# Performance work log

Measured on AMD Instinct MI355X. Metric: run time of the kernel, lower is better.

## Reference

```python
import jax, jax.numpy as jnp
import numpy as np

B, S, D, F, H, E = 4, 1024, 512, 2048, 8, 8
LN_EPS = 1e-5


def setup_inputs() -> dict:
    key = jax.random.key(0)
    ks = jax.random.split(key, 8)
    sd = 1.0 / np.sqrt(D)
    return {
        'x': jax.random.normal(ks[0], (B, S, D), jnp.float32),
        'in_proj_w': jax.random.normal(ks[1], (3 * D, D), jnp.float32) * sd,
        'in_proj_b': jnp.zeros((3 * D,), jnp.float32),
        'out_proj_w': jax.random.normal(ks[2], (D, D), jnp.float32) * sd,
        'out_proj_b': jnp.zeros((D,), jnp.float32),
        'ln1_g': jnp.ones((D,), jnp.float32),
        'ln1_b': jnp.zeros((D,), jnp.float32),
        'ln2_g': jnp.ones((D,), jnp.float32),
        'ln2_b': jnp.zeros((D,), jnp.float32),
        'router_w': jax.random.normal(ks[3], (D, E), jnp.float32) * sd,
        'wi': jax.random.normal(ks[4], (E, D, F), jnp.float32) * sd,
        'wo': jax.random.normal(ks[5], (E, F, D), jnp.float32) * (1.0 / np.sqrt(F)),
        'expert_capacity': 256,
    }


def _layernorm(x, g, b):
    mu = jnp.mean(x, axis=-1, keepdims=True)
    var = jnp.var(x, axis=-1, keepdims=True)
    return (x - mu) * jax.lax.rsqrt(var + LN_EPS) * g + b


def _mha(x, in_w, in_b, out_w, out_b):
    # torch nn.MultiheadAttention, batch_first, self-attention, no mask
    qkv = x @ in_w.T + in_b                         # [B,S,3D]
    q, k, v = jnp.split(qkv, 3, axis=-1)
    hd = D // H

    def heads(t):
        return t.reshape(B, S, H, hd).transpose(0, 2, 1, 3)  # [B,H,S,hd]

    q, k, v = heads(q), heads(k), heads(v)
    scores = jnp.einsum('bhqd,bhkd->bhqk', q, k) / np.sqrt(hd)
    attn = jax.nn.softmax(scores, axis=-1)
    o = jnp.einsum('bhqk,bhkd->bhqd', attn, v)
    o = o.transpose(0, 2, 1, 3).reshape(B, S, D)
    return o @ out_w.T + out_b


def _router(x, router_w, capacity):
    # Switch-style top-1 router with per-(batch,expert) capacity
    logits = x.astype(jnp.float32) @ router_w       # [B,S,E]
    probs = jax.nn.softmax(logits, axis=-1)
    idx = jnp.argmax(probs, axis=-1)                # [B,S]
    one_hot = jax.nn.one_hot(idx, E, dtype=probs.dtype)
    pos = jnp.cumsum(one_hot, axis=1)               # position within each expert queue
    keep = one_hot * (pos <= capacity).astype(probs.dtype)
    expert_mask = keep * probs                      # dispatch mask scaled by router prob
    return expert_mask, probs, logits


def reference(x, in_proj_w, in_proj_b, out_proj_w, out_proj_b,
              ln1_g, ln1_b, ln2_g, ln2_b, router_w, wi, wo, expert_capacity):
    # self-attention block (post-norm)
    residual = x
    a = _mha(x, in_proj_w, in_proj_b, out_proj_w, out_proj_b)
    h = _layernorm(residual + a, ln1_g, ln1_b)

    # sparse MoE FFN
    expert_mask, _, router_logits = _router(h, router_w, expert_capacity)
    residual = h
    moe = jnp.zeros_like(h)
    for e in range(E):  # fixed small expert loop; masked-dense == gather/FFN/scatter
        y = jax.nn.gelu(h @ wi[e], approximate=False) @ wo[e]
        moe = moe + expert_mask[..., e:e + 1] * y

    out = _layernorm(residual + moe, ln2_g, ln2_b)
    return out, router_logits, expert_mask
```

## Files before the change

### kernel.cpp

```cpp
#include <hip/hip_runtime.h>
#include <math.h>

#define SEQ 1024
#define NTOK 4096
#define DM 512
#define FF 2048
#define NE 8

typedef __attribute__((ext_vector_type(8))) short bf16x8;
typedef __attribute__((ext_vector_type(4))) float f32x4;

__device__ __forceinline__ short f2bf(float f) {
  unsigned u = __float_as_uint(f);
  unsigned r = (u + 0x7FFFu + ((u >> 16) & 1u)) >> 16;
  return (short)r;
}
__device__ __forceinline__ float bf2f(short h) {
  return __uint_as_float(((unsigned)(unsigned short)h) << 16);
}

#define GLOAD_LDS16(g, l) __builtin_amdgcn_global_load_lds( \
    (const __attribute__((address_space(1))) void*)(g),     \
    (__attribute__((address_space(3))) void*)(l), 16, 0, 0)

__global__ __launch_bounds__(256) void split_kernel(const float* __restrict__ src,
    short* __restrict__ hi, short* __restrict__ lo) {
  const size_t base = ((size_t)blockIdx.x * 256 + threadIdx.x) * 8;
  float4 v0 = *reinterpret_cast<const float4*>(src + base);
  float4 v1 = *reinterpret_cast<const float4*>(src + base + 4);
  short h[8]; short l[8];
  float v[8] = {v0.x, v0.y, v0.z, v0.w, v1.x, v1.y, v1.z, v1.w};
#pragma unroll
  for (int i = 0; i < 8; ++i) {
    h[i] = f2bf(v[i]);
    l[i] = f2bf(v[i] - bf2f(h[i]));
  }
  *reinterpret_cast<short4*>(hi + base)     = make_short4(h[0], h[1], h[2], h[3]);
  *reinterpret_cast<short4*>(hi + base + 4) = make_short4(h[4], h[5], h[6], h[7]);
  *reinterpret_cast<short4*>(lo + base)     = make_short4(l[0], l[1], l[2], l[3]);
  *reinterpret_cast<short4*>(lo + base + 4) = make_short4(l[4], l[5], l[6], l[7]);
}

template<int BNF>
__global__ __launch_bounds__(256) void gemm_split(const short* __restrict__ Ah, const short* __restrict__ Al,
    const short* __restrict__ Bh, const short* __restrict__ Bl,
    const float* __restrict__ bias, const float* __restrict__ resid, float* __restrict__ C,
    int N, int K) {
  constexpr int BN = 32 * BNF;
  __shared__ __align__(16) short AsH[128 * 32];
  __shared__ __align__(16) short AsL[128 * 32];
  __shared__ __align__(16) short BsH[BN * 32];
  __shared__ __align__(16) short BsL[BN * 32];
  const int n0 = blockIdx.x * BN, m0 = blockIdx.y * 128;
  const int tid = threadIdx.x;
  const int lane = tid & 63, w = tid >> 6;
  const int quad = lane >> 4, l15 = lane & 15;
  const int wm = (w & 1) * 64, wn = (w >> 1) * 16 * BNF;
  const int sr = tid >> 2, sc = (tid & 3) * 8;
  const short* Ahp = Ah + (size_t)(m0 + sr) * K;
  const short* Alp = Al + (size_t)(m0 + sr) * K;
  const short* Bhp = Bh + (size_t)(n0 + sr) * K;
  const short* Blp = Bl + (size_t)(n0 + sr) * K;
  f32x4 acc[4][BNF];
#pragma unroll
  for (int i = 0; i < 4; ++i)
#pragma unroll
    for (int j = 0; j < BNF; ++j) acc[i][j] = (f32x4){0.f, 0.f, 0.f, 0.f};
  for (int kt = 0; kt < K; kt += 32) {
    GLOAD_LDS16(Ahp + kt + sc,                  &AsH[tid * 8]);
    GLOAD_LDS16(Ahp + (size_t)64 * K + kt + sc, &AsH[2048 + tid * 8]);
    GLOAD_LDS16(Alp + kt + sc,                  &AsL[tid * 8]);
    GLOAD_LDS16(Alp + (size_t)64 * K + kt + sc, &AsL[2048 + tid * 8]);
    GLOAD_LDS16(Bhp + kt + sc,                  &BsH[tid * 8]);
    GLOAD_LDS16(Blp + kt + sc,                  &BsL[tid * 8]);
    if (BNF == 4) {
      GLOAD_LDS16(Bhp + (size_t)64 * K + kt + sc, &BsH[2048 + tid * 8]);
      GLOAD_LDS16(Blp + (size_t)64 * K + kt + sc, &BsL[2048 + tid * 8]);
    }
    __syncthreads();
    bf16x8 ah[4], al[4], bh[BNF], bl[BNF];
#pragma unroll
    for (int i = 0; i < 4; ++i) {
      ah[i] = *reinterpret_cast<const bf16x8*>(&AsH[(wm + i * 16 + l15) * 32 + quad * 8]);
      al[i] = *reinterpret_cast<const bf16x8*>(&AsL[(wm + i * 16 + l15) * 32 + quad * 8]);
    }
#pragma unroll
    for (int j = 0; j < BNF; ++j) {
      bh[j] = *reinterpret_cast<const bf16x8*>(&BsH[(wn + j * 16 + l15) * 32 + quad * 8]);
      bl[j] = *reinterpret_cast<const bf16x8*>(&BsL[(wn + j * 16 + l15) * 32 + quad * 8]);
    }
#pragma unroll
    for (int i = 0; i < 4; ++i)
#pragma unroll
      for (int j = 0; j < BNF; ++j) {
        acc[i][j] = __builtin_amdgcn_mfma_f32_16x16x32_bf16(al[i], bh[j], acc[i][j], 0, 0, 0);
        acc[i][j] = __builtin_amdgcn_mfma_f32_16x16x32_bf16(ah[i], bl[j], acc[i][j], 0, 0, 0);
        acc[i][j] = __builtin_amdgcn_mfma_f32_16x16x32_bf16(ah[i], bh[j], acc[i][j], 0, 0, 0);
      }
    __syncthreads();
  }
#pragma unroll
  for (int i = 0; i < 4; ++i) {
#pragma unroll
    for (int reg = 0; reg < 4; ++reg) {
      const int row = m0 + wm + i * 16 + quad * 4 + reg;
#pragma unroll
      for (int j = 0; j < BNF; ++j) {
        const int col = n0 + wn + j * 16 + l15;
        float v = acc[i][j][reg] + bias[col];
        if (resid) v += resid[(size_t)row * N + col];
        C[(size_t)row * N + col] = v;
      }
    }
  }
}

__global__ __launch_bounds__(256) void gemm_split_qkv(const short* __restrict__ Ah, const short* __restrict__ Al,
    const short* __restrict__ Bh, const short* __restrict__ Bl, const float* __restrict__ bias,
    short* __restrict__ qkh, short* __restrict__ qkl, short* __restrict__ vh, short* __restrict__ vl) {
  const int K = DM;
  __shared__ __align__(16) short AsH[128 * 32];
  __shared__ __align__(16) short AsL[128 * 32];
  __shared__ __align__(16) short BsH[128 * 32];
  __shared__ __align__(16) short BsL[128 * 32];
  const int n0 = blockIdx.x * 128, m0 = blockIdx.y * 128;
  const int tid = threadIdx.x;
  const int lane = tid & 63, w = tid >> 6;
  const int quad = lane >> 4, l15 = lane & 15;
  const int wm = (w & 1) * 64, wn = (w >> 1) * 64;
  const int sr = tid >> 2, sc = (tid & 3) * 8;
  const short* Ahp = Ah + (size_t)(m0 + sr) * K;
  const short* Alp = Al + (size_t)(m0 + sr) * K;
  const short* Bhp = Bh + (size_t)(n0 + sr) * K;
  const short* Blp = Bl + (size_t)(n0 + sr) * K;
  f32x4 acc[4][4];
#pragma unroll
  for (int i = 0; i < 4; ++i)
#pragma unroll
    for (int j = 0; j < 4; ++j) acc[i][j] = (f32x4){0.f, 0.f, 0.f, 0.f};
  for (int kt = 0; kt < K; kt += 32) {
    GLOAD_LDS16(Ahp + kt + sc,                  &AsH[tid * 8]);
    GLOAD_LDS16(Ahp + (size_t)64 * K + kt + sc, &AsH[2048 + tid * 8]);
    GLOAD_LDS16(Alp + kt + sc,                  &AsL[tid * 8]);
    GLOAD_LDS16(Alp + (size_t)64 * K + kt + sc, &AsL[2048 + tid * 8]);
    GLOAD_LDS16(Bhp + kt + sc,                  &BsH[tid * 8]);
    GLOAD_LDS16(Bhp + (size_t)64 * K + kt + sc, &BsH[2048 + tid * 8]);
    GLOAD_LDS16(Blp + kt + sc,                  &BsL[tid * 8]);
    GLOAD_LDS16(Blp + (size_t)64 * K + kt + sc, &BsL[2048 + tid * 8]);
    __syncthreads();
    bf16x8 ah[4], al[4], bh[4], bl[4];
#pragma unroll
    for (int i = 0; i < 4; ++i) {
      ah[i] = *reinterpret_cast<const bf16x8*>(&AsH[(wm + i * 16 + l15) * 32 + quad * 8]);
      al[i] = *reinterpret_cast<const bf16x8*>(&AsL[(wm + i * 16 + l15) * 32 + quad * 8]);
      bh[i] = *reinterpret_cast<const bf16x8*>(&BsH[(wn + i * 16 + l15) * 32 + quad * 8]);
      bl[i] = *reinterpret_cast<const bf16x8*>(&BsL[(wn + i * 16 + l15) * 32 + quad * 8]);
    }
#pragma unroll
    for (int i = 0; i < 4; ++i)
#pragma unroll
      for (int j = 0; j < 4; ++j) {
        acc[i][j] = __builtin_amdgcn_mfma_f32_16x16x32_bf16(al[i], bh[j], acc[i][j], 0, 0, 0);
        acc[i][j] = __builtin_amdgcn_mfma_f32_16x16x32_bf16(ah[i], bl[j], acc[i][j], 0, 0, 0);
        acc[i][j] = __builtin_amdgcn_mfma_f32_16x16x32_bf16(ah[i], bh[j], acc[i][j], 0, 0, 0);
      }
    __syncthreads();
  }
  if (blockIdx.x < 8) {
#pragma unroll
    for (int i = 0; i < 4; ++i) {
#pragma unroll
      for (int reg = 0; reg < 4; ++reg) {
        const int row = m0 + wm + i * 16 + quad * 4 + reg;
#pragma unroll
        for (int j = 0; j < 4; ++j) {
          const int col = n0 + wn + j * 16 + l15;
          float v = acc[i][j][reg] + bias[col];
          short hv = f2bf(v);
          size_t ad = (size_t)row * 1024 + col;
          qkh[ad] = hv;
          qkl[ad] = f2bf(v - bf2f(hv));
        }
      }
    }
  } else {
#pragma unroll
    for (int i = 0; i < 4; ++i) {
      const int row0 = m0 + wm + i * 16 + quad * 4;
      const int bb = row0 >> 10, s0 = row0 & 1023;
#pragma unroll
      for (int j = 0; j < 4; ++j) {
        const int col = n0 + wn + j * 16 + l15;
        const int c2 = col - 1024;
        const int hhd = c2 >> 6, d = c2 & 63;
        const float bc = bias[col];
        float v0 = acc[i][j][0] + bc, v1 = acc[i][j][1] + bc, v2 = acc[i][j][2] + bc, v3 = acc[i][j][3] + bc;
        short4 hv = make_short4(f2bf(v0), f2bf(v1), f2bf(v2), f2bf(v3));
        short4 lv = make_short4(f2bf(v0 - bf2f(hv.x)), f2bf(v1 - bf2f(hv.y)),
                                f2bf(v2 - bf2f(hv.z)), f2bf(v3 - bf2f(hv.w)));
        size_t ad = ((size_t)(bb * 8 + hhd) * 64 + d) * 1024 + s0;
        *reinterpret_cast<short4*>(vh + ad) = hv;
        *reinterpret_cast<short4*>(vl + ad) = lv;
      }
    }
  }
}

__global__ __launch_bounds__(256) void attn_mfma(const short* __restrict__ qkh, const short* __restrict__ qkl,
    const short* __restrict__ vth, const short* __restrict__ vtl,
    short* __restrict__ oh, short* __restrict__ ol) {
  const int qt = blockIdx.x, hh = blockIdx.y, b = blockIdx.z;
  __shared__ __align__(16) short Qh[4096], Ql[4096], Kh[4096], Kl[4096], Vh[4096], Vl[4096];
  const int tid = threadIdx.x;
  const int lane = tid & 63, w = tid >> 6;
  const int quad = lane >> 4, l15 = lane & 15;
  const int tok0 = b * SEQ + qt * 64;
  const int srow = tid >> 2, schunk = (tid & 3) * 8;
  {
    const size_t qa = (size_t)(tok0 + srow) * 1024 + hh * 64 + schunk;
    GLOAD_LDS16(qkh + qa,      &Qh[tid * 8]);
    GLOAD_LDS16(qkh + qa + 32, &Qh[2048 + tid * 8]);
    GLOAD_LDS16(qkl + qa,      &Ql[tid * 8]);
    GLOAD_LDS16(qkl + qa + 32, &Ql[2048 + tid * 8]);
  }
  __syncthreads();
  bf16x8 qfh[2], qfl[2];
#pragma unroll
  for (int ks = 0; ks < 2; ++ks) {
    qfh[ks] = *reinterpret_cast<const bf16x8*>(&Qh[ks * 2048 + (w * 16 + l15) * 32 + quad * 8]);
    qfl[ks] = *reinterpret_cast<const bf16x8*>(&Ql[ks * 2048 + (w * 16 + l15) * 32 + quad * 8]);
  }
  f32x4 oacc[4];
  float m_run[4], l_run[4];
#pragma unroll
  for (int r = 0; r < 4; ++r) { oacc[r] = (f32x4){0.f, 0.f, 0.f, 0.f}; m_run[r] = -1e30f; l_run[r] = 0.f; }
  const size_t kbase = (size_t)(b * SEQ) * 1024 + 512 + hh * 64;
  const size_t vbase = (size_t)(b * 8 + hh) * 64 * 1024;
  for (int kc = 0; kc < 16; ++kc) {
    const size_t ka = kbase + (size_t)(kc * 64 + srow) * 1024 + schunk;
    GLOAD_LDS16(qkh + ka,      &Kh[tid * 8]);
    GLOAD_LDS16(qkh + ka + 32, &Kh[2048 + tid * 8]);
    GLOAD_LDS16(qkl + ka,      &Kl[tid * 8]);
    GLOAD_LDS16(qkl + ka + 32, &Kl[2048 + tid * 8]);
    const size_t va = vbase + (size_t)srow * 1024 + kc * 64 + schunk;
    GLOAD_LDS16(vth + va,      &Vh[tid * 8]);
    GLOAD_LDS16(vth + va + 32, &Vh[2048 + tid * 8]);
    GLOAD_LDS16(vtl + va,      &Vl[tid * 8]);
    GLOAD_LDS16(vtl + va + 32, &Vl[2048 + tid * 8]);
    __syncthreads();
    f32x4 s[4];
#pragma unroll
    for (int j = 0; j < 4; ++j) s[j] = (f32x4){0.f, 0.f, 0.f, 0.f};
#pragma unroll
    for (int ks = 0; ks < 2; ++ks)
#pragma unroll
      for (int j = 0; j < 4; ++j) {
        bf16x8 kfh = *reinterpret_cast<const bf16x8*>(&Kh[ks * 2048 + (j * 16 + l15) * 32 + quad * 8]);
        bf16x8 kfl = *reinterpret_cast<const bf16x8*>(&Kl[ks * 2048 + (j * 16 + l15) * 32 + quad * 8]);
        s[j] = __builtin_amdgcn_mfma_f32_16x16x32_bf16(qfl[ks], kfh, s[j], 0, 0, 0);
        s[j] = __builtin_amdgcn_mfma_f32_16x16x32_bf16(qfh[ks], kfl, s[j], 0, 0, 0);
        s[j] = __builtin_amdgcn_mfma_f32_16x16x32_bf16(qfh[ks], kfh, s[j], 0, 0, 0);
      }
    __syncthreads();
    float pv[4][4], alpha[4];
#pragma unroll
    for (int reg = 0; reg < 4; ++reg) {
      float mc = fmaxf(fmaxf(s[0][reg], s[1][reg]), fmaxf(s[2][reg], s[3][reg]));
#pragma unroll
      for (int msk = 1; msk < 16; msk <<= 1) mc = fmaxf(mc, __shfl_xor(mc, msk, 64));
      mc *= 0.125f;
      float mn = fmaxf(m_run[reg], mc);
      alpha[reg] = expf(m_run[reg] - mn);
      m_run[reg] = mn;
      float pl = 0.f;
#pragma unroll
      for (int j = 0; j < 4; ++j) { float pp = expf(s[j][reg] * 0.125f - mn); pv[j][reg] = pp; pl += pp; }
#pragma unroll
      for (int msk = 1; msk < 16; msk <<= 1) pl += __shfl_xor(pl, msk, 64);
      l_run[reg] = l_run[reg] * alpha[reg] + pl;
    }
#pragma unroll
    for (int j = 0; j < 4; ++j) {
      oacc[j][0] *= alpha[0]; oacc[j][1] *= alpha[1]; oacc[j][2] *= alpha[2]; oacc[j][3] *= alpha[3];
    }
#pragma unroll
    for (int j = 0; j < 4; ++j) {
      const int cad = (j >> 1) * 2048 + (j & 1) * 16 + l15;
#pragma unroll
      for (int reg = 0; reg < 4; ++reg) {
        const int ad = cad + (w * 16 + quad * 4 + reg) * 32;
        float p = pv[j][reg];
        short hp = f2bf(p);
        Kh[ad] = hp;
        Kl[ad] = f2bf(p - bf2f(hp));
      }
    }
#pragma unroll
    for (int ks = 0; ks < 2; ++ks) {
      bf16x8 pfh = *reinterpret_cast<const bf16x8*>(&Kh[ks * 2048 + (w * 16 + l15) * 32 + quad * 8]);
      bf16x8 pfl = *reinterpret_cast<const bf16x8*>(&Kl[ks * 2048 + (w * 16 + l15) * 32 + quad * 8]);
#pragma unroll
      for (int j = 0; j < 4; ++j) {
        bf16x8 vfh = *reinterpret_cast<const bf16x8*>(&Vh[ks * 2048 + (j * 16 + l15) * 32 + quad * 8]);
        bf16x8 vfl = *reinterpret_cast<const bf16x8*>(&Vl[ks * 2048 + (j * 16 + l15) * 32 + quad * 8]);
        oacc[j] = __builtin_amdgcn_mfma_f32_16x16x32_bf16(pfl, vfh, oacc[j], 0, 0, 0);
        oacc[j] = __builtin_amdgcn_mfma_f32_16x16x32_bf16(pfh, vfl, oacc[j], 0, 0, 0);
        oacc[j] = __builtin_amdgcn_mfma_f32_16x16x32_bf16(pfh, vfh, oacc[j], 0, 0, 0);
      }
    }
    __syncthreads();
  }
#pragma unroll
  for (int reg = 0; reg < 4; ++reg) {
    float inv = 1.f / l_run[reg];
#pragma unroll
    for (int j = 0; j < 4; ++j) {
      float v = oacc[j][reg] * inv;
      size_t ad = (size_t)(tok0 + w * 16 + quad * 4 + reg) * 512 + hh * 64 + j * 16 + l15;
      short hv = f2bf(v);
      oh[ad] = hv;
      ol[ad] = f2bf(v - bf2f(hv));
    }
  }
}

__global__ __launch_bounds__(64) void ln_kernel(const float* __restrict__ x, const float* __restrict__ add,
    const float* __restrict__ g, const float* __restrict__ bta, float* __restrict__ y) {
  const int t = blockIdx.x, tid = threadIdx.x;
  const size_t base = (size_t)t * DM + tid * 8;
  float4 v0 = *reinterpret_cast<const float4*>(x + base);
  float4 v1 = *reinterpret_cast<const float4*>(x + base + 4);
  if (add) {
    float4 a0 = *reinterpret_cast<const float4*>(add + base);
    float4 a1 = *reinterpret_cast<const float4*>(add + base + 4);
    v0.x += a0.x; v0.y += a0.y; v0.z += a0.z; v0.w += a0.w;
    v1.x += a1.x; v1.y += a1.y; v1.z += a1.z; v1.w += a1.w;
  }
  float s = v0.x+v0.y+v0.z+v0.w + v1.x+v1.y+v1.z+v1.w;
  float q = v0.x*v0.x+v0.y*v0.y+v0.z*v0.z+v0.w*v0.w + v1.x*v1.x+v1.y*v1.y+v1.z*v1.z+v1.w*v1.w;
#pragma unroll
  for (int m = 1; m < 64; m <<= 1) { s += __shfl_xor(s, m, 64); q += __shfl_xor(q, m, 64); }
  float mean = s * (1.0f/512.0f);
  float var = q * (1.0f/512.0f) - mean * mean;
  float rs = rsqrtf(var + 1e-5f);
  float4 g0 = *reinterpret_cast<const float4*>(g + tid*8);
  float4 g1 = *reinterpret_cast<const float4*>(g + tid*8 + 4);
  float4 b0 = *reinterpret_cast<const float4*>(bta + tid*8);
  float4 b1 = *reinterpret_cast<const float4*>(bta + tid*8 + 4);
  float4 o0 = make_float4((v0.x-mean)*rs*g0.x+b0.x, (v0.y-mean)*rs*g0.y+b0.y,
                          (v0.z-mean)*rs*g0.z+b0.z, (v0.w-mean)*rs*g0.w+b0.w);
  float4 o1 = make_float4((v1.x-mean)*rs*g1.x+b1.x, (v1.y-mean)*rs*g1.y+b1.y,
                          (v1.z-mean)*rs*g1.z+b1.z, (v1.w-mean)*rs*g1.w+b1.w);
  *reinterpret_cast<float4*>(y + base) = o0;
  *reinterpret_cast<float4*>(y + base + 4) = o1;
}

__global__ __launch_bounds__(256) void router_kernel(const float* __restrict__ h, const float* __restrict__ rw,
    float* __restrict__ rlog) {
  int gidx = blockIdx.x * 256 + threadIdx.x;
  int t = gidx >> 3, e = gidx & 7;
  const float* hr = h + (size_t)t * DM;
  float acc = 0.f;
#pragma unroll 8
  for (int d = 0; d < DM; ++d) acc += hr[d] * rw[d * NE + e];
  rlog[gidx] = acc;
}

__global__ __launch_bounds__(256) void smax_kernel(const float* __restrict__ rlog, float* __restrict__ probs,
    int* __restrict__ am) {
  int t = blockIdx.x * 256 + threadIdx.x;
  float v[8];
#pragma unroll
  for (int e = 0; e < 8; ++e) v[e] = rlog[t * 8 + e];
  int best = 0; float bv = v[0];
#pragma unroll
  for (int e = 1; e < 8; ++e) if (v[e] > bv) { bv = v[e]; best = e; }
  float ex[8]; float s = 0.f;
#pragma unroll
  for (int e = 0; e < 8; ++e) { ex[e] = expf(v[e] - bv); s += ex[e]; }
  float inv = 1.f / s;
#pragma unroll
  for (int e = 0; e < 8; ++e) probs[t * 8 + e] = ex[e] * inv;
  am[t] = best;
}

__global__ __launch_bounds__(256) void scan_kernel(const int* __restrict__ am, const float* __restrict__ probs,
    const int* __restrict__ capp, float* __restrict__ emask, int* __restrict__ pos, int* __restrict__ cnt) {
  const int bx = blockIdx.x;
  const int b = bx >> 3, e = bx & 7;
  const int tid = threadIdx.x;
  const int cap = *capp;
  __shared__ int arr[256];
  const int s_base = tid * 4;
  int f[4], incl[4];
  int c = 0;
#pragma unroll
  for (int i = 0; i < 4; ++i) {
    f[i] = (am[b * SEQ + s_base + i] == e) ? 1 : 0;
    c += f[i]; incl[i] = c;
  }
  arr[tid] = c;
  __syncthreads();
  for (int off = 1; off < 256; off <<= 1) {
    int v = (tid >= off) ? arr[tid - off] : 0;
    __syncthreads();
    arr[tid] += v;
    __syncthreads();
  }
  int excl = arr[tid] - c;
  int tot = arr[255];
#pragma unroll
  for (int i = 0; i < 4; ++i) {
    int token = b * SEQ + s_base + i;
    int p = excl + incl[i];
    bool kept = f[i] && (p <= cap);
    emask[(size_t)token * NE + e] = kept ? probs[token * NE + e] : 0.f;
    if (f[i]) pos[token] = p;
  }
  if (tid == 0) cnt[bx] = (tot < cap) ? tot : cap;
}

__global__ __launch_bounds__(64) void offsets_kernel(const int* __restrict__ cnt, int* __restrict__ offbe,
    int* __restrict__ total) {
  int e = threadIdx.x;
  if (e < NE) {
    int run = 0;
    for (int b = 0; b < 4; ++b) { offbe[b * NE + e] = run; run += cnt[b * NE + e]; }
    total[e] = run;
  }
}

__global__ __launch_bounds__(256) void transpose_bf16(const float* __restrict__ W, short* __restrict__ Wt,
    int K, int N) {
  __shared__ float T[32][33];
  const float* We = W + (size_t)blockIdx.z * K * N;
  short* Wte = Wt + (size_t)blockIdx.z * K * N;
  const int k0 = blockIdx.y * 32, n0 = blockIdx.x * 32;
  const int r = threadIdx.x >> 3, c4 = (threadIdx.x & 7) * 4;
  float4 v = *reinterpret_cast<const float4*>(&We[(size_t)(k0 + r) * N + n0 + c4]);
  T[r][c4+0] = v.x; T[r][c4+1] = v.y; T[r][c4+2] = v.z; T[r][c4+3] = v.w;
  __syncthreads();
  short4 o;
  o.x = f2bf(T[c4+0][r]); o.y = f2bf(T[c4+1][r]); o.z = f2bf(T[c4+2][r]); o.w = f2bf(T[c4+3][r]);
  *reinterpret_cast<short4*>(&Wte[(size_t)(n0 + r) * K + k0 + c4]) = o;
}

__global__ __launch_bounds__(128) void gather_kernel(const float* __restrict__ h, const int* __restrict__ am,
    const int* __restrict__ pos, const int* __restrict__ capp, const int* __restrict__ offbe,
    const float* __restrict__ probs, short* __restrict__ Gb, int* __restrict__ tok, float* __restrict__ mscale) {
  const int t = blockIdx.x;
  const int b = t >> 10;
  const int e = am[t];
  const int p = pos[t];
  if (p > *capp) return;
  const int slot = offbe[b * NE + e] + p - 1;
  const int idx = e * 1024 + slot;
  if (threadIdx.x == 0) { tok[idx] = t; mscale[idx] = probs[t * NE + e]; }
  float4 v = *reinterpret_cast<const float4*>(h + (size_t)t * DM + threadIdx.x * 4);
  short4 o; o.x = f2bf(v.x); o.y = f2bf(v.y); o.z = f2bf(v.z); o.w = f2bf(v.w);
  *reinterpret_cast<short4*>(Gb + (size_t)idx * DM + threadIdx.x * 4) = o;
}

__global__ __launch_bounds__(256) void ffn1_mfma(const short* __restrict__ Gb, const short* __restrict__ wi_t,
    short* __restrict__ mid, const int* __restrict__ total) {
  const int e = blockIdx.z;
  const int tot = total[e];
  const int m0 = blockIdx.y * 128;
  if (m0 >= tot) return;
  const int n0 = blockIdx.x * 128;
  __shared__ __align__(16) short As[128 * 32];
  __shared__ __align__(16) short Bs[128 * 32];
  const short* A = Gb + ((size_t)e * 1024 + m0) * DM;
  const short* B = wi_t + (size_t)e * FF * DM + (size_t)n0 * DM;
  const int tid = threadIdx.x;
  const int lane = tid & 63, w = tid >> 6;
  const int quad = lane >> 4, l15 = lane & 15;
  const int wm = (w & 1) * 64, wn = (w >> 1) * 64;
  const int sr = tid >> 2, sc = (tid & 3) * 8;
  f32x4 acc[4][4];
#pragma unroll
  for (int i = 0; i < 4; ++i)
#pragma unroll
    for (int j = 0; j < 4; ++j) acc[i][j] = (f32x4){0.f, 0.f, 0.f, 0.f};
  for (int kt = 0; kt < DM; kt += 32) {
    GLOAD_LDS16(A + (size_t)sr * DM + kt + sc,        &As[tid * 8]);
    GLOAD_LDS16(A + (size_t)(sr + 64) * DM + kt + sc, &As[2048 + tid * 8]);
    GLOAD_LDS16(B + (size_t)sr * DM + kt + sc,        &Bs[tid * 8]);
    GLOAD_LDS16(B + (size_t)(sr + 64) * DM + kt + sc, &Bs[2048 + tid * 8]);
    __syncthreads();
    bf16x8 a[4], b[4];
#pragma unroll
    for (int i = 0; i < 4; ++i) a[i] = *reinterpret_cast<const bf16x8*>(&As[(wm + i * 16 + l15) * 32 + quad * 8]);
#pragma unroll
    for (int j = 0; j < 4; ++j) b[j] = *reinterpret_cast<const bf16x8*>(&Bs[(wn + j * 16 + l15) * 32 + quad * 8]);
#pragma unroll
    for (int i = 0; i < 4; ++i)
#pragma unroll
      for (int j = 0; j < 4; ++j)
        acc[i][j] = __builtin_amdgcn_mfma_f32_16x16x32_bf16(a[i], b[j], acc[i][j], 0, 0, 0);
    __syncthreads();
  }
#pragma unroll
  for (int i = 0; i < 4; ++i) {
#pragma unroll
    for (int reg = 0; reg < 4; ++reg) {
      int row = m0 + wm + i * 16 + quad * 4 + reg;
      short* outr = mid + ((size_t)e * 1024 + row) * FF;
#pragma unroll
      for (int j = 0; j < 4; ++j) {
        float v = acc[i][j][reg];
        float gl = 0.5f * v * (1.f + erff(v * 0.70710678118654752f));
        outr[n0 + wn + j * 16 + l15] = f2bf(gl);
      }
    }
  }
}

__global__ __launch_bounds__(256) void ffn2_mfma(const short* __restrict__ mid, const short* __restrict__ wo_t,
    const int* __restrict__ tok, const float* __restrict__ mscale, const int* __restrict__ total,
    float* __restrict__ moebuf) {
  const int e = blockIdx.z;
  const int tot = total[e];
  const int m0 = blockIdx.y * 128;
  if (m0 >= tot) return;
  const int n0 = blockIdx.x * 128;
  __shared__ __align__(16) short As[128 * 32];
  __shared__ __align__(16) short Bs[128 * 32];
  const short* A = mid + ((size_t)e * 1024 + m0) * FF;
  const short* B = wo_t + (size_t)e * DM * FF + (size_t)n0 * FF;
  const int tid = threadIdx.x;
  const int lane = tid & 63, w = tid >> 6;
  const int quad = lane >> 4, l15 = lane & 15;
  const int wm = (w & 1) * 64, wn = (w >> 1) * 64;
  const int sr = tid >> 2, sc = (tid & 3) * 8;
  f32x4 acc[4][4];
#pragma unroll
  for (int i = 0; i < 4; ++i)
#pragma unroll
    for (int j = 0; j < 4; ++j) acc[i][j] = (f32x4){0.f, 0.f, 0.f, 0.f};
  for (int kt = 0; kt < FF; kt += 32) {
    GLOAD_LDS16(A + (size_t)sr * FF + kt + sc,        &As[tid * 8]);
    GLOAD_LDS16(A + (size_t)(sr + 64) * FF + kt + sc, &As[2048 + tid * 8]);
    GLOAD_LDS16(B + (size_t)sr * FF + kt + sc,        &Bs[tid * 8]);
    GLOAD_LDS16(B + (size_t)(sr + 64) * FF + kt + sc, &Bs[2048 + tid * 8]);
    __syncthreads();
    bf16x8 a[4], b[4];
#pragma unroll
    for (int i = 0; i < 4; ++i) a[i] = *reinterpret_cast<const bf16x8*>(&As[(wm + i * 16 + l15) * 32 + quad * 8]);
#pragma unroll
    for (int j = 0; j < 4; ++j) b[j] = *reinterpret_cast<const bf16x8*>(&Bs[(wn + j * 16 + l15) * 32 + quad * 8]);
#pragma unroll
    for (int i = 0; i < 4; ++i)
#pragma unroll
      for (int j = 0; j < 4; ++j)
        acc[i][j] = __builtin_amdgcn_mfma_f32_16x16x32_bf16(a[i], b[j], acc[i][j], 0, 0, 0);
    __syncthreads();
  }
#pragma unroll
  for (int i = 0; i < 4; ++i) {
#pragma unroll
    for (int reg = 0; reg < 4; ++reg) {
      int slot = m0 + wm + i * 16 + quad * 4 + reg;
      if (slot < tot) {
        int idx = e * 1024 + slot;
        int t = tok[idx];
        float scv = mscale[idx];
        float* outr = moebuf + (size_t)t * DM + n0 + wn;
#pragma unroll
        for (int j = 0; j < 4; ++j) outr[j * 16 + l15] = scv * acc[i][j][reg];
      }
    }
  }
}

extern "C" void kernel_launch(void* const* d_in, const int* in_sizes, int n_in,
                              void* d_out, int out_size, void* d_ws, size_t ws_size,
                              hipStream_t stream) {
  const float* x     = (const float*)d_in[0];
  const float* in_w  = (const float*)d_in[1];
  const float* in_b  = (const float*)d_in[2];
  const float* out_w = (const float*)d_in[3];
  const float* out_b = (const float*)d_in[4];
  const float* ln1g  = (const float*)d_in[5];
  const float* ln1b  = (const float*)d_in[6];
  const float* ln2g  = (const float*)d_in[7];
  const float* ln2b  = (const float*)d_in[8];
  const float* rw    = (const float*)d_in[9];
  const float* wi    = (const float*)d_in[10];
  const float* wo    = (const float*)d_in[11];
  const int*   capp  = (const int*)d_in[12];

  float* ws = (float*)d_ws;
  short* qkh  = (short*)ws;
  short* qkl  = (short*)(ws + 2097152);
  short* vth  = (short*)(ws + 4194304);
  short* vtl  = (short*)(ws + 5242880);
  short* Gb16 = (short*)ws;
  short* wi_t = (short*)(ws + 2097152);
  float* moebuf = ws + 6291456;
  float* r1     = ws + 8388608;
  float* h      = ws + 10485760;
  float* probs  = ws + 12582912;
  short* wo_t   = (short*)(ws + 12615680);
  short* mid16  = (short*)(ws + 16809984);
  float* mscale = ws + 25198592;
  int* am    = (int*)(ws + 25206784);
  int* pos   = am + NTOK;
  int* cnt   = pos + NTOK;
  int* offbe = cnt + 32;
  int* total = offbe + 32;
  int* tok   = total + 8;
  short* sAh = (short*)(ws + 25231360);
  short* sAl = sAh + 2097152;
  short* sBh = sAl + 2097152;
  short* sBl = sBh + 786432;

  float* out   = (float*)d_out;
  float* rlog  = out + 2097152;
  float* emask = rlog + 32768;

  split_kernel<<<1024, 256, 0, stream>>>(x, sAh, sAl);
  split_kernel<<<384, 256, 0, stream>>>(in_w, sBh, sBl);
  gemm_split_qkv<<<dim3(12, 32), 256, 0, stream>>>(sAh, sAl, sBh, sBl, in_b, qkh, qkl, vth, vtl);
  attn_mfma<<<dim3(16, 8, 4), 256, 0, stream>>>(qkh, qkl, vth, vtl, sAh, sAl);
  split_kernel<<<128, 256, 0, stream>>>(out_w, sBh, sBl);
  gemm_split<2><<<dim3(8, 32), 256, 0, stream>>>(sAh, sAl, sBh, sBl, out_b, x, r1, DM, DM);
  transpose_bf16<<<dim3(64, 16, 8), 256, 0, stream>>>(wi, wi_t, DM, FF);
  transpose_bf16<<<dim3(16, 64, 8), 256, 0, stream>>>(wo, wo_t, FF, DM);
  ln_kernel<<<NTOK, 64, 0, stream>>>(r1, nullptr, ln1g, ln1b, h);
  router_kernel<<<128, 256, 0, stream>>>(h, rw, rlog);
  smax_kernel<<<16, 256, 0, stream>>>(rlog, probs, am);
  scan_kernel<<<32, 256, 0, stream>>>(am, probs, capp, emask, pos, cnt);
  offsets_kernel<<<1, 64, 0, stream>>>(cnt, offbe, total);
  (void)hipMemsetAsync(moebuf, 0, (size_t)NTOK * DM * sizeof(float), stream);
  gather_kernel<<<NTOK, 128, 0, stream>>>(h, am, pos, capp, offbe, probs, Gb16, tok, mscale);
  ffn1_mfma<<<dim3(16, 8, 8), 256, 0, stream>>>(Gb16, wi_t, mid16, total);
  ffn2_mfma<<<dim3(4, 8, 8), 256, 0, stream>>>(mid16, wo_t, tok, mscale, total, moebuf);
  ln_kernel<<<NTOK, 64, 0, stream>>>(h, moebuf, ln2g, ln2b, out);
}
```

Baseline: 406.9 us.

## Split attention over key halves, fuse LN1 with router, drop MoE memset

Several changes at once. The QKV GEMM uses 128x64 tiles to launch twice as many blocks. Attention is split across two key halves (flash-decoding style), with a new combine kernel merging the partial outputs using the saved max and sum statistics. LayerNorm1, the router matmul and the softmax/argmax are fused into one kernel. The moebuf memset is removed, and the final LayerNorm now adds the MoE output only for tokens kept under capacity. The split attention adds an fp32 partial-output round trip and an extra launch in exchange for more parallelism.

```diff
diff --git a/kernel.cpp b/kernel.cpp
--- a/kernel.cpp
+++ b/kernel.cpp
@@ -121,59 +121,60 @@
   const int K = DM;
   __shared__ __align__(16) short AsH[128 * 32];
   __shared__ __align__(16) short AsL[128 * 32];
-  __shared__ __align__(16) short BsH[128 * 32];
-  __shared__ __align__(16) short BsL[128 * 32];
-  const int n0 = blockIdx.x * 128, m0 = blockIdx.y * 128;
+  __shared__ __align__(16) short BsH[64 * 32];
+  __shared__ __align__(16) short BsL[64 * 32];
+  const int n0 = blockIdx.x * 64, m0 = blockIdx.y * 128;
   const int tid = threadIdx.x;
   const int lane = tid & 63, w = tid >> 6;
   const int quad = lane >> 4, l15 = lane & 15;
-  const int wm = (w & 1) * 64, wn = (w >> 1) * 64;
+  const int wm = (w & 1) * 64, wn = (w >> 1) * 32;
   const int sr = tid >> 2, sc = (tid & 3) * 8;
   const short* Ahp = Ah + (size_t)(m0 + sr) * K;
   const short* Alp = Al + (size_t)(m0 + sr) * K;
   const short* Bhp = Bh + (size_t)(n0 + sr) * K;
   const short* Blp = Bl + (size_t)(n0 + sr) * K;
-  f32x4 acc[4][4];
+  f32x4 acc[4][2];
 #pragma unroll
   for (int i = 0; i < 4; ++i)
 #pragma unroll
-    for (int j = 0; j < 4; ++j) acc[i][j] = (f32x4){0.f, 0.f, 0.f, 0.f};
+    for (int j = 0; j < 2; ++j) acc[i][j] = (f32x4){0.f, 0.f, 0.f, 0.f};
   for (int kt = 0; kt < K; kt += 32) {
     GLOAD_LDS16(Ahp + kt + sc,                  &AsH[tid * 8]);
     GLOAD_LDS16(Ahp + (size_t)64 * K + kt + sc, &AsH[2048 + tid * 8]);
     GLOAD_LDS16(Alp + kt + sc,                  &AsL[tid * 8]);
     GLOAD_LDS16(Alp + (size_t)64 * K + kt + sc, &AsL[2048 + tid * 8]);
     GLOAD_LDS16(Bhp + kt + sc,                  &BsH[tid * 8]);
-    GLOAD_LDS16(Bhp + (size_t)64 * K + kt + sc, &BsH[2048 + tid * 8]);
     GLOAD_LDS16(Blp + kt + sc,                  &BsL[tid * 8]);
-    GLOAD_LDS16(Blp + (size_t)64 * K + kt + sc, &BsL[2048 + tid * 8]);
-    __syncthreads();
-    bf16x8 ah[4], al[4], bh[4], bl[4];
+    __syncthreads();
+    bf16x8 ah[4], al[4], bh[2], bl[2];
 #pragma unroll
     for (int i = 0; i < 4; ++i) {
       ah[i] = *reinterpret_cast<const bf16x8*>(&AsH[(wm + i * 16 + l15) * 32 + quad * 8]);
       al[i] = *reinterpret_cast<const bf16x8*>(&AsL[(wm + i * 16 + l15) * 32 + quad * 8]);
-      bh[i] = *reinterpret_cast<const bf16x8*>(&BsH[(wn + i * 16 + l15) * 32 + quad * 8]);
-      bl[i] = *reinterpret_cast<const bf16x8*>(&BsL[(wn + i * 16 + l15) * 32 + quad * 8]);
+    }
+#pragma unroll
+    for (int j = 0; j < 2; ++j) {
+      bh[j] = *reinterpret_cast<const bf16x8*>(&BsH[(wn + j * 16 + l15) * 32 + quad * 8]);
+      bl[j] = *reinterpret_cast<const bf16x8*>(&BsL[(wn + j * 16 + l15) * 32 + quad * 8]);
     }
 #pragma unroll
     for (int i = 0; i < 4; ++i)
 #pragma unroll
-      for (int j = 0; j < 4; ++j) {
+      for (int j = 0; j < 2; ++j) {
         acc[i][j] = __builtin_amdgcn_mfma_f32_16x16x32_bf16(al[i], bh[j], acc[i][j], 0, 0, 0);
         acc[i][j] = __builtin_amdgcn_mfma_f32_16x16x32_bf16(ah[i], bl[j], acc[i][j], 0, 0, 0);
         acc[i][j] = __builtin_amdgcn_mfma_f32_16x16x32_bf16(ah[i], bh[j], acc[i][j], 0, 0, 0);
       }
     __syncthreads();
   }
-  if (blockIdx.x < 8) {
+  if (n0 < 1024) {
 #pragma unroll
     for (int i = 0; i < 4; ++i) {
 #pragma unroll
       for (int reg = 0; reg < 4; ++reg) {
         const int row = m0 + wm + i * 16 + quad * 4 + reg;
 #pragma unroll
-        for (int j = 0; j < 4; ++j) {
+        for (int j = 0; j < 2; ++j) {
           const int col = n0 + wn + j * 16 + l15;
           float v = acc[i][j][reg] + bias[col];
           short hv = f2bf(v);
@@ -189,7 +190,7 @@
       const int row0 = m0 + wm + i * 16 + quad * 4;
       const int bb = row0 >> 10, s0 = row0 & 1023;
 #pragma unroll
-      for (int j = 0; j < 4; ++j) {
+      for (int j = 0; j < 2; ++j) {
         const int col = n0 + wn + j * 16 + l15;
         const int c2 = col - 1024;
         const int hhd = c2 >> 6, d = c2 & 63;
@@ -208,8 +209,9 @@
 
 __global__ __launch_bounds__(256) void attn_mfma(const short* __restrict__ qkh, const short* __restrict__ qkl,
     const short* __restrict__ vth, const short* __restrict__ vtl,
-    short* __restrict__ oh, short* __restrict__ ol) {
-  const int qt = blockIdx.x, hh = blockIdx.y, b = blockIdx.z;
+    float* __restrict__ opart, float* __restrict__ ml) {
+  const int qt = blockIdx.x, hh = blockIdx.y;
+  const int b = blockIdx.z >> 1, ks = blockIdx.z & 1;
   __shared__ __align__(16) short Qh[4096], Ql[4096], Kh[4096], Kl[4096], Vh[4096], Vl[4096];
   const int tid = threadIdx.x;
   const int lane = tid & 63, w = tid >> 6;
@@ -226,9 +228,9 @@
   __syncthreads();
   bf16x8 qfh[2], qfl[2];
 #pragma unroll
-  for (int ks = 0; ks < 2; ++ks) {
-    qfh[ks] = *reinterpret_cast<const bf16x8*>(&Qh[ks * 2048 + (w * 16 + l15) * 32 + quad * 8]);
-    qfl[ks] = *reinterpret_cast<const bf16x8*>(&Ql[ks * 2048 + (w * 16 + l15) * 32 + quad * 8]);
+  for (int kk = 0; kk < 2; ++kk) {
+    qfh[kk] = *reinterpret_cast<const bf16x8*>(&Qh[kk * 2048 + (w * 16 + l15) * 32 + quad * 8]);
+    qfl[kk] = *reinterpret_cast<const bf16x8*>(&Ql[kk * 2048 + (w * 16 + l15) * 32 + quad * 8]);
   }
   f32x4 oacc[4];
   float m_run[4], l_run[4];
@@ -236,7 +238,7 @@
   for (int r = 0; r < 4; ++r) { oacc[r] = (f32x4){0.f, 0.f, 0.f, 0.f}; m_run[r] = -1e30f; l_run[r] = 0.f; }
   const size_t kbase = (size_t)(b * SEQ) * 1024 + 512 + hh * 64;
   const size_t vbase = (size_t)(b * 8 + hh) * 64 * 1024;
-  for (int kc = 0; kc < 16; ++kc) {
+  for (int kc = ks * 8; kc < ks * 8 + 8; ++kc) {
     const size_t ka = kbase + (size_t)(kc * 64 + srow) * 1024 + schunk;
     GLOAD_LDS16(qkh + ka,      &Kh[tid * 8]);
     GLOAD_LDS16(qkh + ka + 32, &Kh[2048 + tid * 8]);
@@ -252,14 +254,14 @@
 #pragma unroll
     for (int j = 0; j < 4; ++j) s[j] = (f32x4){0.f, 0.f, 0.f, 0.f};
 #pragma unroll
-    for (int ks = 0; ks < 2; ++ks)
+    for (int kk = 0; kk < 2; ++kk)
 #pragma unroll
       for (int j = 0; j < 4; ++j) {
-        bf16x8 kfh = *reinterpret_cast<const bf16x8*>(&Kh[ks * 2048 + (j * 16 + l15) * 32 + quad * 8]);
-        bf16x8 kfl = *reinterpret_cast<const bf16x8*>(&Kl[ks * 2048 + (j * 16 + l15) * 32 + quad * 8]);
-        s[j] = __builtin_amdgcn_mfma_f32_16x16x32_bf16(qfl[ks], kfh, s[j], 0, 0, 0);
-        s[j] = __builtin_amdgcn_mfma_f32_16x16x32_bf16(qfh[ks], kfl, s[j], 0, 0, 0);
-        s[j] = __builtin_amdgcn_mfma_f32_16x16x32_bf16(qfh[ks], kfh, s[j], 0, 0, 0);
+        bf16x8 kfh = *reinterpret_cast<const bf16x8*>(&Kh[kk * 2048 + (j * 16 + l15) * 32 + quad * 8]);
+        bf16x8 kfl = *reinterpret_cast<const bf16x8*>(&Kl[kk * 2048 + (j * 16 + l15) * 32 + quad * 8]);
+        s[j] = __builtin_amdgcn_mfma_f32_16x16x32_bf16(qfl[kk], kfh, s[j], 0, 0, 0);
+        s[j] = __builtin_amdgcn_mfma_f32_16x16x32_bf16(qfh[kk], kfl, s[j], 0, 0, 0);
+        s[j] = __builtin_amdgcn_mfma_f32_16x16x32_bf16(qfh[kk], kfh, s[j], 0, 0, 0);
       }
     __syncthreads();
     float pv[4][4], alpha[4];
@@ -296,13 +298,13 @@
       }
     }
 #pragma unroll
-    for (int ks = 0; ks < 2; ++ks) {
-      bf16x8 pfh = *reinterpret_cast<const bf16x8*>(&Kh[ks * 2048 + (w * 16 + l15) * 32 + quad * 8]);
-      bf16x8 pfl = *reinterpret_cast<const bf16x8*>(&Kl[ks * 2048 + (w * 16 + l15) * 32 + quad * 8]);
+    for (int kk = 0; kk < 2; ++kk) {
+      bf16x8 pfh = *reinterpret_cast<const bf16x8*>(&Kh[kk * 2048 + (w * 16 + l15) * 32 + quad * 8]);
+      bf16x8 pfl = *reinterpret_cast<const bf16x8*>(&Kl[kk * 2048 + (w * 16 + l15) * 32 + quad * 8]);
 #pragma unroll
       for (int j = 0; j < 4; ++j) {
-        bf16x8 vfh = *reinterpret_cast<const bf16x8*>(&Vh[ks * 2048 + (j * 16 + l15) * 32 + quad * 8]);
-        bf16x8 vfl = *reinterpret_cast<const bf16x8*>(&Vl[ks * 2048 + (j * 16 + l15) * 32 + quad * 8]);
+        bf16x8 vfh = *reinterpret_cast<const bf16x8*>(&Vh[kk * 2048 + (j * 16 + l15) * 32 + quad * 8]);
+        bf16x8 vfl = *reinterpret_cast<const bf16x8*>(&Vl[kk * 2048 + (j * 16 + l15) * 32 + quad * 8]);
         oacc[j] = __builtin_amdgcn_mfma_f32_16x16x32_bf16(pfl, vfh, oacc[j], 0, 0, 0);
         oacc[j] = __builtin_amdgcn_mfma_f32_16x16x32_bf16(pfh, vfl, oacc[j], 0, 0, 0);
         oacc[j] = __builtin_amdgcn_mfma_f32_16x16x32_bf16(pfh, vfh, oacc[j], 0, 0, 0);
@@ -310,27 +312,104 @@
     }
     __syncthreads();
   }
+  float* op = opart + (size_t)ks * 2097152;
 #pragma unroll
   for (int reg = 0; reg < 4; ++reg) {
-    float inv = 1.f / l_run[reg];
-#pragma unroll
-    for (int j = 0; j < 4; ++j) {
-      float v = oacc[j][reg] * inv;
-      size_t ad = (size_t)(tok0 + w * 16 + quad * 4 + reg) * 512 + hh * 64 + j * 16 + l15;
-      short hv = f2bf(v);
-      oh[ad] = hv;
-      ol[ad] = f2bf(v - bf2f(hv));
-    }
-  }
-}
-
-__global__ __launch_bounds__(64) void ln_kernel(const float* __restrict__ x, const float* __restrict__ add,
+    const int rloc = w * 16 + quad * 4 + reg;
+#pragma unroll
+    for (int j = 0; j < 4; ++j)
+      op[(size_t)(tok0 + rloc) * 512 + hh * 64 + j * 16 + l15] = oacc[j][reg];
+    if (l15 == 0) {
+      size_t mli = (((size_t)ks * 32 + b * 8 + hh) * 1024 + qt * 64 + rloc) * 2;
+      ml[mli] = m_run[reg];
+      ml[mli + 1] = l_run[reg];
+    }
+  }
+}
+
+__global__ __launch_bounds__(64) void combine_attn(const float* __restrict__ opart, const float* __restrict__ ml,
+    short* __restrict__ oh, short* __restrict__ ol) {
+  const int t = blockIdx.x;
+  const int b = t >> 10, s = t & 1023;
+  const int tid = threadIdx.x;
+#pragma unroll
+  for (int hh = 0; hh < 8; ++hh) {
+    size_t mli = (((size_t)(b * 8 + hh)) * 1024 + s) * 2;
+    float m0 = ml[mli], l0 = ml[mli + 1];
+    float m1 = ml[65536 + mli], l1 = ml[65536 + mli + 1];
+    float mm = fmaxf(m0, m1);
+    float a0 = expf(m0 - mm), a1 = expf(m1 - mm);
+    float inv = 1.f / (l0 * a0 + l1 * a1);
+    size_t ad = (size_t)t * 512 + hh * 64 + tid;
+    float v = (opart[ad] * a0 + opart[2097152 + ad] * a1) * inv;
+    short hv = f2bf(v);
+    oh[ad] = hv;
+    ol[ad] = f2bf(v - bf2f(hv));
+  }
+}
+
+__global__ __launch_bounds__(64) void ln_router(const float* __restrict__ r1,
+    const float* __restrict__ g, const float* __restrict__ bta, const float* __restrict__ rw,
+    float* __restrict__ h, float* __restrict__ rlog, float* __restrict__ probs, int* __restrict__ am) {
+  const int t = blockIdx.x, tid = threadIdx.x;
+  const size_t base = (size_t)t * DM + tid * 8;
+  float4 v0 = *reinterpret_cast<const float4*>(r1 + base);
+  float4 v1 = *reinterpret_cast<const float4*>(r1 + base + 4);
+  float s = v0.x+v0.y+v0.z+v0.w + v1.x+v1.y+v1.z+v1.w;
+  float q = v0.x*v0.x+v0.y*v0.y+v0.z*v0.z+v0.w*v0.w + v1.x*v1.x+v1.y*v1.y+v1.z*v1.z+v1.w*v1.w;
+#pragma unroll
+  for (int m = 1; m < 64; m <<= 1) { s += __shfl_xor(s, m, 64); q += __shfl_xor(q, m, 64); }
+  float mean = s * (1.0f/512.0f);
+  float var = q * (1.0f/512.0f) - mean * mean;
+  float rs = rsqrtf(var + 1e-5f);
+  float4 g0 = *reinterpret_cast<const float4*>(g + tid*8);
+  float4 g1 = *reinterpret_cast<const float4*>(g + tid*8 + 4);
+  float4 b0 = *reinterpret_cast<const float4*>(bta + tid*8);
+  float4 b1 = *reinterpret_cast<const float4*>(bta + tid*8 + 4);
+  float hv[8];
+  hv[0] = (v0.x-mean)*rs*g0.x+b0.x; hv[1] = (v0.y-mean)*rs*g0.y+b0.y;
+  hv[2] = (v0.z-mean)*rs*g0.z+b0.z; hv[3] = (v0.w-mean)*rs*g0.w+b0.w;
+  hv[4] = (v1.x-mean)*rs*g1.x+b1.x; hv[5] = (v1.y-mean)*rs*g1.y+b1.y;
+  hv[6] = (v1.z-mean)*rs*g1.z+b1.z; hv[7] = (v1.w-mean)*rs*g1.w+b1.w;
+  *reinterpret_cast<float4*>(h + base)     = make_float4(hv[0], hv[1], hv[2], hv[3]);
+  *reinterpret_cast<float4*>(h + base + 4) = make_float4(hv[4], hv[5], hv[6], hv[7]);
+  float lg[8] = {0.f,0.f,0.f,0.f,0.f,0.f,0.f,0.f};
+  const float* rwp = rw + tid * 64;
+#pragma unroll
+  for (int r = 0; r < 8; ++r) {
+    float4 w0 = *reinterpret_cast<const float4*>(rwp + r * 8);
+    float4 w1 = *reinterpret_cast<const float4*>(rwp + r * 8 + 4);
+    float hr = hv[r];
+    lg[0] += hr * w0.x; lg[1] += hr * w0.y; lg[2] += hr * w0.z; lg[3] += hr * w0.w;
+    lg[4] += hr * w1.x; lg[5] += hr * w1.y; lg[6] += hr * w1.z; lg[7] += hr * w1.w;
+  }
+#pragma unroll
+  for (int m = 1; m < 64; m <<= 1) {
+#pragma unroll
+    for (int e = 0; e < 8; ++e) lg[e] += __shfl_xor(lg[e], m, 64);
+  }
+  int best = 0; float bv = lg[0];
+#pragma unroll
+  for (int e = 1; e < 8; ++e) if (lg[e] > bv) { bv = lg[e]; best = e; }
+  float se = 0.f;
+#pragma unroll
+  for (int e = 0; e < 8; ++e) se += expf(lg[e] - bv);
+  float inv = 1.f / se;
+  if (tid < 8) {
+    rlog[t * 8 + tid] = lg[tid];
+    probs[t * 8 + tid] = expf(lg[tid] - bv) * inv;
+  }
+  if (tid == 0) am[t] = best;
+}
+
+__global__ __launch_bounds__(64) void ln2_kernel(const float* __restrict__ x, const float* __restrict__ add,
+    const int* __restrict__ pos, const int* __restrict__ capp,
     const float* __restrict__ g, const float* __restrict__ bta, float* __restrict__ y) {
   const int t = blockIdx.x, tid = threadIdx.x;
   const size_t base = (size_t)t * DM + tid * 8;
   float4 v0 = *reinterpret_cast<const float4*>(x + base);
   float4 v1 = *reinterpret_cast<const float4*>(x + base + 4);
-  if (add) {
+  if (pos[t] <= *capp) {
     float4 a0 = *reinterpret_cast<const float4*>(add + base);
     float4 a1 = *reinterpret_cast<const float4*>(add + base + 4);
     v0.x += a0.x; v0.y += a0.y; v0.z += a0.z; v0.w += a0.w;
@@ -353,35 +432,6 @@
                           (v1.z-mean)*rs*g1.z+b1.z, (v1.w-mean)*rs*g1.w+b1.w);
   *reinterpret_cast<float4*>(y + base) = o0;
   *reinterpret_cast<float4*>(y + base + 4) = o1;
-}
-
-__global__ __launch_bounds__(256) void router_kernel(const float* __restrict__ h, const float* __restrict__ rw,
-    float* __restrict__ rlog) {
-  int gidx = blockIdx.x * 256 + threadIdx.x;
-  int t = gidx >> 3, e = gidx & 7;
-  const float* hr = h + (size_t)t * DM;
-  float acc = 0.f;
-#pragma unroll 8
-  for (int d = 0; d < DM; ++d) acc += hr[d] * rw[d * NE + e];
-  rlog[gidx] = acc;
-}
-
-__global__ __launch_bounds__(256) void smax_kernel(const float* __restrict__ rlog, float* __restrict__ probs,
-    int* __restrict__ am) {
-  int t = blockIdx.x * 256 + threadIdx.x;
-  float v[8];
-#pragma unroll
-  for (int e = 0; e < 8; ++e) v[e] = rlog[t * 8 + e];
-  int best = 0; float bv = v[0];
-#pragma unroll
-  for (int e = 1; e < 8; ++e) if (v[e] > bv) { bv = v[e]; best = e; }
-  float ex[8]; float s = 0.f;
-#pragma unroll
-  for (int e = 0; e < 8; ++e) { ex[e] = expf(v[e] - bv); s += ex[e]; }
-  float inv = 1.f / s;
-#pragma unroll
-  for (int e = 0; e < 8; ++e) probs[t * 8 + e] = ex[e] * inv;
-  am[t] = best;
 }
 
 __global__ __launch_bounds__(256) void scan_kernel(const int* __restrict__ am, const float* __restrict__ probs,
@@ -602,6 +652,8 @@
   float* h      = ws + 10485760;
   float* probs  = ws + 12582912;
   short* wo_t   = (short*)(ws + 12615680);
+  float* opart  = ws + 16809984;
+  float* mlbuf  = ws + 16809984 + 4194304;
   short* mid16  = (short*)(ws + 16809984);
   float* mscale = ws + 25198592;
   int* am    = (int*)(ws + 25206784);
@@ -621,20 +673,18 @@
 
   split_kernel<<<1024, 256, 0, stream>>>(x, sAh, sAl);
   split_kernel<<<384, 256, 0, stream>>>(in_w, sBh, sBl);
-  gemm_split_qkv<<<dim3(12, 32), 256, 0, stream>>>(sAh, sAl, sBh, sBl, in_b, qkh, qkl, vth, vtl);
-  attn_mfma<<<dim3(16, 8, 4), 256, 0, stream>>>(qkh, qkl, vth, vtl, sAh, sAl);
+  gemm_split_qkv<<<dim3(24, 32), 256, 0, stream>>>(sAh, sAl, sBh, sBl, in_b, qkh, qkl, vth, vtl);
+  attn_mfma<<<dim3(16, 8, 8), 256, 0, stream>>>(qkh, qkl, vth, vtl, opart, mlbuf);
+  combine_attn<<<NTOK, 64, 0, stream>>>(opart, mlbuf, sAh, sAl);
   split_kernel<<<128, 256, 0, stream>>>(out_w, sBh, sBl);
   gemm_split<2><<<dim3(8, 32), 256, 0, stream>>>(sAh, sAl, sBh, sBl, out_b, x, r1, DM, DM);
   transpose_bf16<<<dim3(64, 16, 8), 256, 0, stream>>>(wi, wi_t, DM, FF);
   transpose_bf16<<<dim3(16, 64, 8), 256, 0, stream>>>(wo, wo_t, FF, DM);
-  ln_kernel<<<NTOK, 64, 0, stream>>>(r1, nullptr, ln1g, ln1b, h);
-  router_kernel<<<128, 256, 0, stream>>>(h, rw, rlog);
-  smax_kernel<<<16, 256, 0, stream>>>(rlog, probs, am);
+  ln_router<<<NTOK, 64, 0, stream>>>(r1, ln1g, ln1b, rw, h, rlog, probs, am);
   scan_kernel<<<32, 256, 0, stream>>>(am, probs, capp, emask, pos, cnt);
   offsets_kernel<<<1, 64, 0, stream>>>(cnt, offbe, total);
-  (void)hipMemsetAsync(moebuf, 0, (size_t)NTOK * DM * sizeof(float), stream);
   gather_kernel<<<NTOK, 128, 0, stream>>>(h, am, pos, capp, offbe, probs, Gb16, tok, mscale);
   ffn1_mfma<<<dim3(16, 8, 8), 256, 0, stream>>>(Gb16, wi_t, mid16, total);
   ffn2_mfma<<<dim3(4, 8, 8), 256, 0, stream>>>(mid16, wo_t, tok, mscale, total, moebuf);
-  ln_kernel<<<NTOK, 64, 0, stream>>>(h, moebuf, ln2g, ln2b, out);
-}
+  ln2_kernel<<<NTOK, 64, 0, stream>>>(h, moebuf, pos, capp, ln2g, ln2b, out);
+}
```

After: 372.2 us. 8.5% less time.
